# Optimization experiments

Measured on AMD Instinct MI355X. Metric: run time of the kernel, lower is better.

The kernel has to match this reference:

```python
import jax, jax.numpy as jnp
import numpy as np

B, L, H, O, N = 64, 2048, 128, 128, 256  # batch, window, num_states, num_actions, dynamics state dim


def setup_inputs() -> dict:
    key = jax.random.key(0)
    ks = jax.random.split(key, 12)
    # LRU-style stable init: |lambda| in (r_min, r_max)
    u1 = jax.random.uniform(ks[0], (N,))
    u2 = jax.random.uniform(ks[1], (N,))
    r_min, r_max = 0.4, 0.99
    nu_log = jnp.log(-0.5 * jnp.log(u1 * (r_max**2 - r_min**2) + r_min**2))
    theta_log = jnp.log(u2 * 2.0 * jnp.pi)
    lam_abs2 = jnp.exp(-2.0 * jnp.exp(nu_log))
    gamma_log = 0.5 * jnp.log(1.0 - lam_abs2)  # gamma normalization
    return {
        "state": jax.random.normal(ks[2], (B, H), jnp.float32),
        "dynamics_input_time_window": jax.random.normal(ks[3], (B, L, H), jnp.float32),
        "dynamics_disturbance_time_window": jax.random.normal(ks[4], (B, L, H), jnp.float32),
        "nu_log": nu_log.astype(jnp.float32),
        "theta_log": theta_log.astype(jnp.float32),
        "gamma_log": gamma_log.astype(jnp.float32),
        "B_re": jax.random.normal(ks[5], (N, H), jnp.float32) / np.sqrt(2 * H),
        "B_im": jax.random.normal(ks[6], (N, H), jnp.float32) / np.sqrt(2 * H),
        "C_re": jax.random.normal(ks[7], (O, N), jnp.float32) / np.sqrt(N),
        "C_im": jax.random.normal(ks[8], (O, N), jnp.float32) / np.sqrt(N),
        "D": jax.random.normal(ks[9], (O, H), jnp.float32) / np.sqrt(H),
    }


def _ssm_scan(u, nu_log, theta_log, gamma_log, B_re, B_im, C_re, C_im, D):
    # u: [B, L, H] real. Diagonal complex LRU: x_t = lam * x_{t-1} + gamma*B u_t; y = Re(C x) + D u
    lam = jnp.exp(-jnp.exp(nu_log) + 1j * jnp.exp(theta_log))           # [N]
    Bmat = (B_re + 1j * B_im) * jnp.exp(gamma_log)[:, None]              # [N, H]
    Bu = jnp.einsum("blh,nh->bln", u.astype(jnp.complex64), Bmat)       # [B, L, N]
    lam_seq = jnp.broadcast_to(lam, Bu.shape)

    def comb(e1, e2):
        a1, b1 = e1
        a2, b2 = e2
        return a1 * a2, a2 * b1 + b2

    _, x = jax.lax.associative_scan(comb, (lam_seq, Bu), axis=1)        # [B, L, N]
    y = jnp.einsum("bln,on->blo", x, C_re + 1j * C_im).real
    y = y + jnp.einsum("blh,oh->blo", u, D)
    return y


def reference(state, dynamics_input_time_window, dynamics_disturbance_time_window,
              nu_log, theta_log, gamma_log, B_re, B_im, C_re, C_im, D):
    # 3-dim branch of Actor.forward: run SSM over the disturbance window, take last step
    y = _ssm_scan(dynamics_disturbance_time_window, nu_log, theta_log, gamma_log,
                  B_re, B_im, C_re, C_im, D)                             # [B, L, O]
    action = y[:, -1, :]                                                 # [B, O]
    return action
```

## Files before the change

### kernel.cpp

```cpp
#include <hip/hip_runtime.h>
#include <hip/hip_bf16.h>
#include <math.h>
#include <stdint.h>

#define B_ 64
#define L_ 2048
#define H_ 128
#define O_ 128
#define N_ 256
#define CH_ 128
#define NCH_ 16
#define SPC_ 8

using f32x4 = __attribute__((ext_vector_type(4))) float;
using i32x4 = __attribute__((ext_vector_type(4))) int;
using h16x8 = __attribute__((ext_vector_type(8))) _Float16;

__device__ __forceinline__ unsigned short f16_bits(float v) {
    _Float16 h = (_Float16)v;
    return __builtin_bit_cast(unsigned short, h);
}
__device__ __forceinline__ int pack_f16(float a, float b) {
    return (int)((unsigned)f16_bits(a) | ((unsigned)f16_bits(b) << 16));
}

__global__ void prep_kernel(const float* __restrict__ nu_log, const float* __restrict__ theta_log,
                            const float* __restrict__ gamma_log, const float* __restrict__ B_re,
                            const float* __restrict__ B_im, unsigned short* __restrict__ B2Tr,
                            float2* __restrict__ lamjR, float2* __restrict__ lam16R,
                            float2* __restrict__ lamCCr, float* __restrict__ nuR,
                            int* __restrict__ perm, float* __restrict__ X) {
    __shared__ float nu_s[N_];
    __shared__ int perm_s[N_];
    const int t = threadIdx.x;
    float nu = expf(nu_log[t]);
    nu_s[t] = nu;
    __syncthreads();
    {
        int rank = 0;
        for (int j = 0; j < N_; ++j) {
            float vj = nu_s[j];
            rank += (vj < nu || (vj == nu && j < t)) ? 1 : 0;
        }
        perm_s[rank] = t;
    }
    __syncthreads();
    const int bb = blockIdx.x;
    if (bb < 64) {
        #pragma unroll
        for (int kk = 0; kk < 4; ++kk) {
            int e = bb * 1024 + kk * 256 + t;
            int part = e >> 15, rank = (e >> 7) & 255, h = e & 127;
            int n = perm_s[rank];
            float g = expf(gamma_log[n]);
            float v = (part ? B_im : B_re)[n * H_ + h] * g;
            B2Tr[e] = f16_bits(v);
        }
    } else if (bb == 64) {
        int r = t, n = perm_s[r];
        float nun = nu_s[n];
        double th = (double)expf(theta_log[n]);
        double rr = exp(-(double)nun);
        double sn, cs;
        sincos(th, &sn, &cs);
        double lre = rr * cs, lim = rr * sn;
        double pre = 1.0, pim = 0.0;
        for (int k = 0; k < 16; ++k) {
            lamjR[r * 16 + 15 - k] = make_float2((float)pre, (float)pim);
            double t1 = pre * lre - pim * lim, t2 = pre * lim + pim * lre;
            pre = t1; pim = t2;
        }
        lam16R[r] = make_float2((float)pre, (float)pim);
        nuR[r] = nun;
        perm[r] = n;
        double wre = pre, wim = pim;
        for (int i = 0; i < 3; ++i) {
            double a = wre * wre - wim * wim, b2 = 2.0 * wre * wim;
            wre = a; wim = b2;
        }
        double are = 1.0, aim = 0.0;
        for (int c = 15; c >= 0; --c) {
            lamCCr[c * N_ + r] = make_float2((float)are, (float)aim);
            double a = are * wre - aim * wim, b2 = are * wim + aim * wre;
            are = a; aim = b2;
        }
    } else {
        int idx = (bb - 65) * 1024 + t * 4;
        f32x4 z = {0.f, 0.f, 0.f, 0.f};
        *(f32x4*)&X[idx] = z;
    }
}

__global__ __launch_bounds__(256, 2)
void scan_kernel(const float* __restrict__ u, const unsigned short* __restrict__ B2Tr,
                 const float2* __restrict__ lamjR, const float2* __restrict__ lam16R,
                 const float2* __restrict__ lamCCr, const float* __restrict__ nuR,
                 const int* __restrict__ perm, float* __restrict__ X) {
    const int half = blockIdx.x & 1;
    const int c = (blockIdx.x >> 1) & 15;
    const int b = (int)(blockIdx.x >> 5);
    const int tid = threadIdx.x;
    const int wave = tid >> 6, lane = tid & 63;
    const int m = lane & 15, q = lane >> 4;
    const int g = half * 4 + wave;

    const float base_e = 2032.0f - 128.0f * (float)c;
    int sblk = (int)ceilf((base_e - 35.0f / nuR[half * 128]) * 0.0625f);
    if (sblk >= SPC_) return;
    if (sblk < 0) sblk = 0;
    int sp0 = (int)ceilf((base_e - 35.0f / nuR[g * 32]) * 0.0625f);
    if (sp0 < 0) sp0 = 0;
    int sp1 = (int)ceilf((base_e - 35.0f / nuR[g * 32 + 16]) * 0.0625f);
    if (sp1 < 0) sp1 = 0;

    __shared__ __align__(16) unsigned short ubuf[2][16 * 128];

    h16x8 bf[2][2][4];
    float2 wl[2][4];
    float2 l16[2];
    #pragma unroll
    for (int p = 0; p < 2; ++p) {
        const int rank = g * 32 + p * 16 + m;
        #pragma unroll
        for (int part = 0; part < 2; ++part) {
            const unsigned short* rp = B2Tr + (size_t)(part * N_ + rank) * H_ + q * 8;
            #pragma unroll
            for (int sl = 0; sl < 4; ++sl)
                bf[p][part][sl] = *(const h16x8*)(rp + sl * 32);
        }
        #pragma unroll
        for (int r = 0; r < 4; ++r) wl[p][r] = lamjR[rank * 16 + q * 4 + r];
        l16[p] = lam16R[rank];
    }

    float2 zr[2], zi[2];
    #pragma unroll
    for (int p = 0; p < 2; ++p) { zr[p] = make_float2(0.f, 0.f); zi[p] = make_float2(0.f, 0.f); }

    const int sr = tid >> 4, sg = tid & 15;
    const float* gsrc = u + ((size_t)b * L_ + (size_t)c * CH_) * H_;
    const float* gstage = gsrc + (size_t)sr * H_ + sg * 8;
    unsigned short* lwr = &ubuf[0][0] + sr * 128 + ((sg ^ sr) * 8);
    const int bufStride = 16 * 128;

    {
        const float* p4 = gstage + (size_t)sblk * 16 * H_;
        float4 a = *(const float4*)p4, b4 = *(const float4*)(p4 + 4);
        i32x4 w;
        w[0] = pack_f16(a.x, a.y);  w[1] = pack_f16(a.z, a.w);
        w[2] = pack_f16(b4.x, b4.y); w[3] = pack_f16(b4.z, b4.w);
        *(i32x4*)(lwr + (sblk & 1) * bufStride) = w;
    }
    __syncthreads();

    for (int s = sblk; s < SPC_; ++s) {
        const bool pf = (s + 1 < SPC_);
        float4 a, b4;
        if (pf) {
            const float* p4 = gstage + (size_t)(s + 1) * 16 * H_;
            a = *(const float4*)p4;
            b4 = *(const float4*)(p4 + 4);
        }

        const unsigned short* lb = &ubuf[s & 1][0];
        h16x8 afr[4];
        #pragma unroll
        for (int sl = 0; sl < 4; ++sl) {
            const int unit = (sl * 4 + q) ^ m;
            afr[sl] = *(const h16x8*)(lb + m * 128 + unit * 8);
        }

        #pragma unroll
        for (int p = 0; p < 2; ++p) {
            const int sp = p ? sp1 : sp0;
            if (s < sp) continue;
            float2 t0 = zr[p];
            zr[p].x = l16[p].x * t0.x - l16[p].y * t0.y;
            zr[p].y = l16[p].x * t0.y + l16[p].y * t0.x;
            float2 t1 = zi[p];
            zi[p].x = l16[p].x * t1.x - l16[p].y * t1.y;
            zi[p].y = l16[p].x * t1.y + l16[p].y * t1.x;
            f32x4 acc = {0.f, 0.f, 0.f, 0.f};
            #pragma unroll
            for (int sl = 0; sl < 4; ++sl)
                acc = __builtin_amdgcn_mfma_f32_16x16x32_f16(afr[sl], bf[p][0][sl], acc, 0, 0, 0);
            #pragma unroll
            for (int r = 0; r < 4; ++r) {
                zr[p].x += wl[p][r].x * acc[r];
                zr[p].y += wl[p][r].y * acc[r];
            }
            f32x4 acc2 = {0.f, 0.f, 0.f, 0.f};
            #pragma unroll
            for (int sl = 0; sl < 4; ++sl)
                acc2 = __builtin_amdgcn_mfma_f32_16x16x32_f16(afr[sl], bf[p][1][sl], acc2, 0, 0, 0);
            #pragma unroll
            for (int r = 0; r < 4; ++r) {
                zi[p].x += wl[p][r].x * acc2[r];
                zi[p].y += wl[p][r].y * acc2[r];
            }
        }

        if (pf) {
            i32x4 w;
            w[0] = pack_f16(a.x, a.y);  w[1] = pack_f16(a.z, a.w);
            w[2] = pack_f16(b4.x, b4.y); w[3] = pack_f16(b4.z, b4.w);
            *(i32x4*)(lwr + ((s + 1) & 1) * bufStride) = w;
        }
        __syncthreads();
    }

    #pragma unroll
    for (int p = 0; p < 2; ++p) {
        const int sp = p ? sp1 : sp0;
        if (sp >= SPC_) continue;
        float a = zr[p].x, b2 = zr[p].y, c2 = zi[p].x, d2 = zi[p].y;
        a  += __shfl_xor(a, 16);  a  += __shfl_xor(a, 32);
        b2 += __shfl_xor(b2, 16); b2 += __shfl_xor(b2, 32);
        c2 += __shfl_xor(c2, 16); c2 += __shfl_xor(c2, 32);
        d2 += __shfl_xor(d2, 16); d2 += __shfl_xor(d2, 32);
        if (lane < 16) {
            const int rank = g * 32 + p * 16 + m;
            const int n = perm[rank];
            float2 lc = lamCCr[c * N_ + rank];
            float prr = lc.x * a - lc.y * b2;
            float pri = lc.x * b2 + lc.y * a;
            float pir = lc.x * c2 - lc.y * d2;
            float pii = lc.x * d2 + lc.y * c2;
            atomicAdd(&X[(size_t)(b * N_ + n) * 2 + 0], prr - pii);
            atomicAdd(&X[(size_t)(b * N_ + n) * 2 + 1], pri + pir);
        }
    }
}

__global__ void out_kernel(const float* __restrict__ X, const float* __restrict__ C_re,
                           const float* __restrict__ C_im, const float* __restrict__ Dm,
                           const float* __restrict__ u, float* __restrict__ out) {
    __shared__ float xre[N_], xim[N_], ul[H_];
    const int b = blockIdx.x;
    const int t = threadIdx.x;
    xre[t] = X[(size_t)(b * N_ + t) * 2 + 0];
    xim[t] = X[(size_t)(b * N_ + t) * 2 + 1];
    if (t < H_) ul[t] = u[((size_t)b * L_ + (L_ - 1)) * H_ + t];
    __syncthreads();
    const int o = t >> 1;
    const int h = t & 1;
    const float* cre = C_re + o * N_ + h * 128;
    const float* cim = C_im + o * N_ + h * 128;
    const float* xr = xre + h * 128;
    const float* xi = xim + h * 128;
    float s = 0.f;
    #pragma unroll 4
    for (int n = 0; n < 128; ++n) s += cre[n] * xr[n] - cim[n] * xi[n];
    const float* dp = Dm + o * H_ + h * 64;
    const float* up = ul + h * 64;
    #pragma unroll 4
    for (int k = 0; k < 64; ++k) s += dp[k] * up[k];
    s += __shfl_xor(s, 1);
    if (h == 0) out[b * O_ + o] = s;
}

extern "C" void kernel_launch(void* const* d_in, const int* in_sizes, int n_in,
                              void* d_out, int out_size, void* d_ws, size_t ws_size,
                              hipStream_t stream) {
    const float* u         = (const float*)d_in[2];
    const float* nu_log    = (const float*)d_in[3];
    const float* theta_log = (const float*)d_in[4];
    const float* gamma_log = (const float*)d_in[5];
    const float* B_re      = (const float*)d_in[6];
    const float* B_im      = (const float*)d_in[7];
    const float* C_re      = (const float*)d_in[8];
    const float* C_im      = (const float*)d_in[9];
    const float* Dm        = (const float*)d_in[10];

    char* ws = (char*)d_ws;
    float*          X      = (float*)ws;
    unsigned short* B2Tr   = (unsigned short*)(ws + 131072);
    float2*         lamjR  = (float2*)(ws + 262144);
    float2*         lam16R = (float2*)(ws + 294912);
    float2*         lamCCr = (float2*)(ws + 296960);
    float*          nuR    = (float*)(ws + 329728);
    int*            perm   = (int*)(ws + 330752);

    prep_kernel<<<97, 256, 0, stream>>>(nu_log, theta_log, gamma_log, B_re, B_im,
                                        B2Tr, lamjR, lam16R, lamCCr, nuR, perm, X);
    scan_kernel<<<B_ * NCH_ * 2, 256, 0, stream>>>(u, B2Tr, lamjR, lam16R, lamCCr, nuR, perm, X);
    out_kernel<<<B_, 256, 0, stream>>>(X, C_re, C_im, Dm, u, (float*)d_out);
}
```

Before: 193.4 us.

## Deepen global prefetch to three stages with register ring and raise occupancy bound

```diff
diff --git a/kernel.cpp b/kernel.cpp
--- a/kernel.cpp
+++ b/kernel.cpp
@@ -91,7 +91,7 @@
     }
 }
 
-__global__ __launch_bounds__(256, 2)
+__global__ __launch_bounds__(256, 3)
 void scan_kernel(const float* __restrict__ u, const unsigned short* __restrict__ B2Tr,
                  const float2* __restrict__ lamjR, const float2* __restrict__ lam16R,
                  const float2* __restrict__ lamCCr, const float* __restrict__ nuR,
@@ -112,6 +112,7 @@
     if (sp0 < 0) sp0 = 0;
     int sp1 = (int)ceilf((base_e - 35.0f / nuR[g * 32 + 16]) * 0.0625f);
     if (sp1 < 0) sp1 = 0;
+    const int live = SPC_ - sblk;
 
     __shared__ __align__(16) unsigned short ubuf[2][16 * 128];
 
@@ -138,31 +139,38 @@
     for (int p = 0; p < 2; ++p) { zr[p] = make_float2(0.f, 0.f); zi[p] = make_float2(0.f, 0.f); }
 
     const int sr = tid >> 4, sg = tid & 15;
-    const float* gsrc = u + ((size_t)b * L_ + (size_t)c * CH_) * H_;
-    const float* gstage = gsrc + (size_t)sr * H_ + sg * 8;
+    const float* gbase = u + ((size_t)b * L_ + (size_t)(c * CH_ + sblk * 16)) * H_
+                           + (size_t)sr * H_ + sg * 8;
     unsigned short* lwr = &ubuf[0][0] + sr * 128 + ((sg ^ sr) * 8);
     const int bufStride = 16 * 128;
 
+    float4 ra[3], rb[3];
+    #pragma unroll
+    for (int k = 0; k < 3; ++k) {
+        if (k < live) {
+            const float* p4 = gbase + (size_t)k * 16 * H_;
+            ra[k] = *(const float4*)p4;
+            rb[k] = *(const float4*)(p4 + 4);
+        }
+    }
     {
-        const float* p4 = gstage + (size_t)sblk * 16 * H_;
-        float4 a = *(const float4*)p4, b4 = *(const float4*)(p4 + 4);
         i32x4 w;
-        w[0] = pack_f16(a.x, a.y);  w[1] = pack_f16(a.z, a.w);
-        w[2] = pack_f16(b4.x, b4.y); w[3] = pack_f16(b4.z, b4.w);
-        *(i32x4*)(lwr + (sblk & 1) * bufStride) = w;
-    }
-    __syncthreads();
-
-    for (int s = sblk; s < SPC_; ++s) {
-        const bool pf = (s + 1 < SPC_);
-        float4 a, b4;
-        if (pf) {
-            const float* p4 = gstage + (size_t)(s + 1) * 16 * H_;
-            a = *(const float4*)p4;
-            b4 = *(const float4*)(p4 + 4);
-        }
-
-        const unsigned short* lb = &ubuf[s & 1][0];
+        w[0] = pack_f16(ra[0].x, ra[0].y);  w[1] = pack_f16(ra[0].z, ra[0].w);
+        w[2] = pack_f16(rb[0].x, rb[0].y);  w[3] = pack_f16(rb[0].z, rb[0].w);
+        *(i32x4*)lwr = w;
+    }
+    __syncthreads();
+
+    #pragma unroll
+    for (int i = 0; i < SPC_; ++i) {
+        if (i >= live) break;
+        if (i + 3 < live) {
+            const float* p4 = gbase + (size_t)(i + 3) * 16 * H_;
+            ra[(i + 3) % 3] = *(const float4*)p4;
+            rb[(i + 3) % 3] = *(const float4*)(p4 + 4);
+        }
+
+        const unsigned short* lb = &ubuf[i & 1][0];
         h16x8 afr[4];
         #pragma unroll
         for (int sl = 0; sl < 4; ++sl) {
@@ -170,6 +178,15 @@
             afr[sl] = *(const h16x8*)(lb + m * 128 + unit * 8);
         }
 
+        if (i + 1 < live) {
+            const int sl3 = (i + 1) % 3;
+            i32x4 w;
+            w[0] = pack_f16(ra[sl3].x, ra[sl3].y);  w[1] = pack_f16(ra[sl3].z, ra[sl3].w);
+            w[2] = pack_f16(rb[sl3].x, rb[sl3].y);  w[3] = pack_f16(rb[sl3].z, rb[sl3].w);
+            *(i32x4*)(lwr + ((i + 1) & 1) * bufStride) = w;
+        }
+
+        const int s = sblk + i;
         #pragma unroll
         for (int p = 0; p < 2; ++p) {
             const int sp = p ? sp1 : sp0;
@@ -198,13 +215,6 @@
                 zi[p].x += wl[p][r].x * acc2[r];
                 zi[p].y += wl[p][r].y * acc2[r];
             }
-        }
-
-        if (pf) {
-            i32x4 w;
-            w[0] = pack_f16(a.x, a.y);  w[1] = pack_f16(a.z, a.w);
-            w[2] = pack_f16(b4.x, b4.y); w[3] = pack_f16(b4.z, b4.w);
-            *(i32x4*)(lwr + ((s + 1) & 1) * bufStride) = w;
         }
         __syncthreads();
     }
```

Measured after the change: 197.0 us. About the same (+1.9%).

## Deepen global-load prefetch in scan kernel, remap block order, raise occupancy

Applied to the files above, without the earlier changes.

```diff
diff --git a/kernel.cpp b/kernel.cpp
--- a/kernel.cpp
+++ b/kernel.cpp
@@ -23,6 +23,8 @@
 __device__ __forceinline__ int pack_f16(float a, float b) {
     return (int)((unsigned)f16_bits(a) | ((unsigned)f16_bits(b) << 16));
 }
+
+#define BAR_LDS() asm volatile("s_waitcnt lgkmcnt(0)\n\ts_barrier" ::: "memory")
 
 __global__ void prep_kernel(const float* __restrict__ nu_log, const float* __restrict__ theta_log,
                             const float* __restrict__ gamma_log, const float* __restrict__ B_re,
@@ -91,14 +93,15 @@
     }
 }
 
-__global__ __launch_bounds__(256, 2)
+__global__ __launch_bounds__(256, 4)
 void scan_kernel(const float* __restrict__ u, const unsigned short* __restrict__ B2Tr,
                  const float2* __restrict__ lamjR, const float2* __restrict__ lam16R,
                  const float2* __restrict__ lamCCr, const float* __restrict__ nuR,
                  const int* __restrict__ perm, float* __restrict__ X) {
-    const int half = blockIdx.x & 1;
-    const int c = (blockIdx.x >> 1) & 15;
-    const int b = (int)(blockIdx.x >> 5);
+    const int bx = blockIdx.x;
+    const int half = bx >> 10;
+    const int c = (bx >> 6) & 15;
+    const int b = bx & 63;
     const int tid = threadIdx.x;
     const int wave = tid >> 6, lane = tid & 63;
     const int m = lane & 15, q = lane >> 4;
@@ -112,6 +115,7 @@
     if (sp0 < 0) sp0 = 0;
     int sp1 = (int)ceilf((base_e - 35.0f / nuR[g * 32 + 16]) * 0.0625f);
     if (sp1 < 0) sp1 = 0;
+    const int live = SPC_ - sblk;
 
     __shared__ __align__(16) unsigned short ubuf[2][16 * 128];
 
@@ -138,38 +142,27 @@
     for (int p = 0; p < 2; ++p) { zr[p] = make_float2(0.f, 0.f); zi[p] = make_float2(0.f, 0.f); }
 
     const int sr = tid >> 4, sg = tid & 15;
-    const float* gsrc = u + ((size_t)b * L_ + (size_t)c * CH_) * H_;
-    const float* gstage = gsrc + (size_t)sr * H_ + sg * 8;
+    const float* gbase = u + ((size_t)b * L_ + (size_t)(c * CH_ + sblk * 16)) * H_
+                           + (size_t)sr * H_ + sg * 8;
     unsigned short* lwr = &ubuf[0][0] + sr * 128 + ((sg ^ sr) * 8);
     const int bufStride = 16 * 128;
 
-    {
-        const float* p4 = gstage + (size_t)sblk * 16 * H_;
-        float4 a = *(const float4*)p4, b4 = *(const float4*)(p4 + 4);
-        i32x4 w;
-        w[0] = pack_f16(a.x, a.y);  w[1] = pack_f16(a.z, a.w);
-        w[2] = pack_f16(b4.x, b4.y); w[3] = pack_f16(b4.z, b4.w);
-        *(i32x4*)(lwr + (sblk & 1) * bufStride) = w;
-    }
-    __syncthreads();
-
-    for (int s = sblk; s < SPC_; ++s) {
-        const bool pf = (s + 1 < SPC_);
-        float4 a, b4;
-        if (pf) {
-            const float* p4 = gstage + (size_t)(s + 1) * 16 * H_;
-            a = *(const float4*)p4;
-            b4 = *(const float4*)(p4 + 4);
-        }
-
-        const unsigned short* lb = &ubuf[s & 1][0];
+    float4 a0, b0, a1, b1, a2, b2;
+
+#define LOADS(slot, idx) { const float* p4_ = gbase + (size_t)(idx) * (16 * H_); \
+        a##slot = *(const float4*)p4_; b##slot = *(const float4*)(p4_ + 4); }
+#define STORES(slot, bufi) { i32x4 w_; \
+        w_[0] = pack_f16(a##slot.x, a##slot.y);  w_[1] = pack_f16(a##slot.z, a##slot.w); \
+        w_[2] = pack_f16(b##slot.x, b##slot.y);  w_[3] = pack_f16(b##slot.z, b##slot.w); \
+        *(i32x4*)(lwr + (bufi) * bufStride) = w_; }
+
+    auto compute = [&](const unsigned short* lb, int s) {
         h16x8 afr[4];
         #pragma unroll
         for (int sl = 0; sl < 4; ++sl) {
             const int unit = (sl * 4 + q) ^ m;
             afr[sl] = *(const h16x8*)(lb + m * 128 + unit * 8);
         }
-
         #pragma unroll
         for (int p = 0; p < 2; ++p) {
             const int sp = p ? sp1 : sp0;
@@ -199,15 +192,33 @@
                 zi[p].y += wl[p][r].y * acc2[r];
             }
         }
-
-        if (pf) {
-            i32x4 w;
-            w[0] = pack_f16(a.x, a.y);  w[1] = pack_f16(a.z, a.w);
-            w[2] = pack_f16(b4.x, b4.y); w[3] = pack_f16(b4.z, b4.w);
-            *(i32x4*)(lwr + ((s + 1) & 1) * bufStride) = w;
-        }
-        __syncthreads();
-    }
+    };
+
+    LOADS(0, 0);
+    if (1 < live) LOADS(1, 1);
+    if (2 < live) LOADS(2, 2);
+    STORES(0, 0);
+    BAR_LDS();
+
+#define ITER(i, lslot, wslot) \
+    if ((i) < live) { \
+        if ((i) + 3 < live) LOADS(lslot, (i) + 3); \
+        if ((i) + 1 < live) STORES(wslot, ((i) + 1) & 1); \
+        compute(&ubuf[(i) & 1][0], sblk + (i)); \
+        BAR_LDS(); \
+    }
+
+    ITER(0, 0, 1)
+    ITER(1, 1, 2)
+    ITER(2, 2, 0)
+    ITER(3, 0, 1)
+    ITER(4, 1, 2)
+    ITER(5, 2, 0)
+    ITER(6, 0, 1)
+    ITER(7, 1, 2)
+#undef ITER
+#undef LOADS
+#undef STORES
 
     #pragma unroll
     for (int p = 0; p < 2; ++p) {
```

Result: slower. 238.2 us (+23.2%).

## Stage whole chunk in LDS once and run per-wave independent scans

Applied to the files above, without the earlier changes.

```diff
diff --git a/kernel.cpp b/kernel.cpp
--- a/kernel.cpp
+++ b/kernel.cpp
@@ -91,143 +91,118 @@
     }
 }
 
-__global__ __launch_bounds__(256, 2)
+__global__ __launch_bounds__(512, 4)
 void scan_kernel(const float* __restrict__ u, const unsigned short* __restrict__ B2Tr,
                  const float2* __restrict__ lamjR, const float2* __restrict__ lam16R,
                  const float2* __restrict__ lamCCr, const float* __restrict__ nuR,
                  const int* __restrict__ perm, float* __restrict__ X) {
-    const int half = blockIdx.x & 1;
-    const int c = (blockIdx.x >> 1) & 15;
-    const int b = (int)(blockIdx.x >> 5);
+    const int bx = blockIdx.x;
+    const int c = bx & 15;
+    const int b = bx >> 4;
     const int tid = threadIdx.x;
-    const int wave = tid >> 6, lane = tid & 63;
+
+    __shared__ __align__(16) unsigned short Asm[CH_ * H_];
+
+    {
+        const int r = tid >> 2;
+        const int qq = tid & 3;
+        const float* gsrc = u + ((size_t)b * L_ + (size_t)(c * CH_ + r)) * H_ + qq * 32;
+        f32x4 Lv[8];
+        #pragma unroll
+        for (int k = 0; k < 8; ++k) Lv[k] = *(const f32x4*)(gsrc + k * 4);
+        #pragma unroll
+        for (int j = 0; j < 4; ++j) {
+            const int unit = (qq * 4 + j) ^ (r & 15);
+            i32x4 w;
+            w[0] = pack_f16(Lv[2 * j][0], Lv[2 * j][1]);
+            w[1] = pack_f16(Lv[2 * j][2], Lv[2 * j][3]);
+            w[2] = pack_f16(Lv[2 * j + 1][0], Lv[2 * j + 1][1]);
+            w[3] = pack_f16(Lv[2 * j + 1][2], Lv[2 * j + 1][3]);
+            *(i32x4*)&Asm[r * H_ + unit * 8] = w;
+        }
+    }
+    __syncthreads();
+
+    const int g = tid >> 6;
+    const int lane = tid & 63;
     const int m = lane & 15, q = lane >> 4;
-    const int g = half * 4 + wave;
 
     const float base_e = 2032.0f - 128.0f * (float)c;
-    int sblk = (int)ceilf((base_e - 35.0f / nuR[half * 128]) * 0.0625f);
-    if (sblk >= SPC_) return;
-    if (sblk < 0) sblk = 0;
     int sp0 = (int)ceilf((base_e - 35.0f / nuR[g * 32]) * 0.0625f);
     if (sp0 < 0) sp0 = 0;
     int sp1 = (int)ceilf((base_e - 35.0f / nuR[g * 32 + 16]) * 0.0625f);
     if (sp1 < 0) sp1 = 0;
 
-    __shared__ __align__(16) unsigned short ubuf[2][16 * 128];
-
-    h16x8 bf[2][2][4];
-    float2 wl[2][4];
-    float2 l16[2];
-    #pragma unroll
-    for (int p = 0; p < 2; ++p) {
-        const int rank = g * 32 + p * 16 + m;
-        #pragma unroll
-        for (int part = 0; part < 2; ++part) {
-            const unsigned short* rp = B2Tr + (size_t)(part * N_ + rank) * H_ + q * 8;
-            #pragma unroll
-            for (int sl = 0; sl < 4; ++sl)
-                bf[p][part][sl] = *(const h16x8*)(rp + sl * 32);
-        }
-        #pragma unroll
-        for (int r = 0; r < 4; ++r) wl[p][r] = lamjR[rank * 16 + q * 4 + r];
-        l16[p] = lam16R[rank];
-    }
-
-    float2 zr[2], zi[2];
-    #pragma unroll
-    for (int p = 0; p < 2; ++p) { zr[p] = make_float2(0.f, 0.f); zi[p] = make_float2(0.f, 0.f); }
-
-    const int sr = tid >> 4, sg = tid & 15;
-    const float* gsrc = u + ((size_t)b * L_ + (size_t)c * CH_) * H_;
-    const float* gstage = gsrc + (size_t)sr * H_ + sg * 8;
-    unsigned short* lwr = &ubuf[0][0] + sr * 128 + ((sg ^ sr) * 8);
-    const int bufStride = 16 * 128;
-
-    {
-        const float* p4 = gstage + (size_t)sblk * 16 * H_;
-        float4 a = *(const float4*)p4, b4 = *(const float4*)(p4 + 4);
-        i32x4 w;
-        w[0] = pack_f16(a.x, a.y);  w[1] = pack_f16(a.z, a.w);
-        w[2] = pack_f16(b4.x, b4.y); w[3] = pack_f16(b4.z, b4.w);
-        *(i32x4*)(lwr + (sblk & 1) * bufStride) = w;
-    }
-    __syncthreads();
-
-    for (int s = sblk; s < SPC_; ++s) {
-        const bool pf = (s + 1 < SPC_);
-        float4 a, b4;
-        if (pf) {
-            const float* p4 = gstage + (size_t)(s + 1) * 16 * H_;
-            a = *(const float4*)p4;
-            b4 = *(const float4*)(p4 + 4);
-        }
-
-        const unsigned short* lb = &ubuf[s & 1][0];
-        h16x8 afr[4];
-        #pragma unroll
-        for (int sl = 0; sl < 4; ++sl) {
-            const int unit = (sl * 4 + q) ^ m;
-            afr[sl] = *(const h16x8*)(lb + m * 128 + unit * 8);
-        }
-
+    if (sp0 < SPC_) {
         #pragma unroll
         for (int p = 0; p < 2; ++p) {
             const int sp = p ? sp1 : sp0;
-            if (s < sp) continue;
-            float2 t0 = zr[p];
-            zr[p].x = l16[p].x * t0.x - l16[p].y * t0.y;
-            zr[p].y = l16[p].x * t0.y + l16[p].y * t0.x;
-            float2 t1 = zi[p];
-            zi[p].x = l16[p].x * t1.x - l16[p].y * t1.y;
-            zi[p].y = l16[p].x * t1.y + l16[p].y * t1.x;
-            f32x4 acc = {0.f, 0.f, 0.f, 0.f};
+            if (sp >= SPC_) continue;
+            const int rank = g * 32 + p * 16 + m;
+
+            h16x8 bfr[2][4];
             #pragma unroll
-            for (int sl = 0; sl < 4; ++sl)
-                acc = __builtin_amdgcn_mfma_f32_16x16x32_f16(afr[sl], bf[p][0][sl], acc, 0, 0, 0);
+            for (int part = 0; part < 2; ++part) {
+                const unsigned short* rp = B2Tr + (size_t)(part * N_ + rank) * H_ + q * 8;
+                #pragma unroll
+                for (int sl = 0; sl < 4; ++sl)
+                    bfr[part][sl] = *(const h16x8*)(rp + sl * 32);
+            }
+            float2 wl[4];
             #pragma unroll
-            for (int r = 0; r < 4; ++r) {
-                zr[p].x += wl[p][r].x * acc[r];
-                zr[p].y += wl[p][r].y * acc[r];
+            for (int r2 = 0; r2 < 4; ++r2) wl[r2] = lamjR[rank * 16 + q * 4 + r2];
+            const float2 l16 = lam16R[rank];
+
+            float2 zre = make_float2(0.f, 0.f), zim = make_float2(0.f, 0.f);
+            for (int s = sp; s < SPC_; ++s) {
+                const int row = s * 16 + m;
+                h16x8 afr[4];
+                #pragma unroll
+                for (int sl = 0; sl < 4; ++sl) {
+                    const int unit = (sl * 4 + q) ^ m;
+                    afr[sl] = *(const h16x8*)&Asm[row * H_ + unit * 8];
+                }
+                float2 t0 = zre;
+                zre.x = l16.x * t0.x - l16.y * t0.y;
+                zre.y = l16.x * t0.y + l16.y * t0.x;
+                float2 t1 = zim;
+                zim.x = l16.x * t1.x - l16.y * t1.y;
+                zim.y = l16.x * t1.y + l16.y * t1.x;
+                f32x4 acc = {0.f, 0.f, 0.f, 0.f};
+                #pragma unroll
+                for (int sl = 0; sl < 4; ++sl)
+                    acc = __builtin_amdgcn_mfma_f32_16x16x32_f16(afr[sl], bfr[0][sl], acc, 0, 0, 0);
+                #pragma unroll
+                for (int r2 = 0; r2 < 4; ++r2) {
+                    zre.x += wl[r2].x * acc[r2];
+                    zre.y += wl[r2].y * acc[r2];
+                }
+                f32x4 acc2 = {0.f, 0.f, 0.f, 0.f};
+                #pragma unroll
+                for (int sl = 0; sl < 4; ++sl)
+                    acc2 = __builtin_amdgcn_mfma_f32_16x16x32_f16(afr[sl], bfr[1][sl], acc2, 0, 0, 0);
+                #pragma unroll
+                for (int r2 = 0; r2 < 4; ++r2) {
+                    zim.x += wl[r2].x * acc2[r2];
+                    zim.y += wl[r2].y * acc2[r2];
+                }
             }
-            f32x4 acc2 = {0.f, 0.f, 0.f, 0.f};
-            #pragma unroll
-            for (int sl = 0; sl < 4; ++sl)
-                acc2 = __builtin_amdgcn_mfma_f32_16x16x32_f16(afr[sl], bf[p][1][sl], acc2, 0, 0, 0);
-            #pragma unroll
-            for (int r = 0; r < 4; ++r) {
-                zi[p].x += wl[p][r].x * acc2[r];
-                zi[p].y += wl[p][r].y * acc2[r];
+
+            float a = zre.x, b2 = zre.y, c2 = zim.x, d2 = zim.y;
+            a  += __shfl_xor(a, 16);  a  += __shfl_xor(a, 32);
+            b2 += __shfl_xor(b2, 16); b2 += __shfl_xor(b2, 32);
+            c2 += __shfl_xor(c2, 16); c2 += __shfl_xor(c2, 32);
+            d2 += __shfl_xor(d2, 16); d2 += __shfl_xor(d2, 32);
+            if (lane < 16) {
+                const int n = perm[rank];
+                float2 lc = lamCCr[c * N_ + rank];
+                float prr = lc.x * a - lc.y * b2;
+                float pri = lc.x * b2 + lc.y * a;
+                float pir = lc.x * c2 - lc.y * d2;
+                float pii = lc.x * d2 + lc.y * c2;
+                atomicAdd(&X[(size_t)(b * N_ + n) * 2 + 0], prr - pii);
+                atomicAdd(&X[(size_t)(b * N_ + n) * 2 + 1], pri + pir);
             }
-        }
-
-        if (pf) {
-            i32x4 w;
-            w[0] = pack_f16(a.x, a.y);  w[1] = pack_f16(a.z, a.w);
-            w[2] = pack_f16(b4.x, b4.y); w[3] = pack_f16(b4.z, b4.w);
-            *(i32x4*)(lwr + ((s + 1) & 1) * bufStride) = w;
-        }
-        __syncthreads();
-    }
-
-    #pragma unroll
-    for (int p = 0; p < 2; ++p) {
-        const int sp = p ? sp1 : sp0;
-        if (sp >= SPC_) continue;
-        float a = zr[p].x, b2 = zr[p].y, c2 = zi[p].x, d2 = zi[p].y;
-        a  += __shfl_xor(a, 16);  a  += __shfl_xor(a, 32);
-        b2 += __shfl_xor(b2, 16); b2 += __shfl_xor(b2, 32);
-        c2 += __shfl_xor(c2, 16); c2 += __shfl_xor(c2, 32);
-        d2 += __shfl_xor(d2, 16); d2 += __shfl_xor(d2, 32);
-        if (lane < 16) {
-            const int rank = g * 32 + p * 16 + m;
-            const int n = perm[rank];
-            float2 lc = lamCCr[c * N_ + rank];
-            float prr = lc.x * a - lc.y * b2;
-            float pri = lc.x * b2 + lc.y * a;
-            float pir = lc.x * c2 - lc.y * d2;
-            float pii = lc.x * d2 + lc.y * c2;
-            atomicAdd(&X[(size_t)(b * N_ + n) * 2 + 0], prr - pii);
-            atomicAdd(&X[(size_t)(b * N_ + n) * 2 + 1], pri + pir);
         }
     }
 }
@@ -283,6 +258,6 @@
 
     prep_kernel<<<97, 256, 0, stream>>>(nu_log, theta_log, gamma_log, B_re, B_im,
                                         B2Tr, lamjR, lam16R, lamCCr, nuR, perm, X);
-    scan_kernel<<<B_ * NCH_ * 2, 256, 0, stream>>>(u, B2Tr, lamjR, lam16R, lamCCr, nuR, perm, X);
+    scan_kernel<<<B_ * NCH_, 512, 0, stream>>>(u, B2Tr, lamjR, lam16R, lamCCr, nuR, perm, X);
     out_kernel<<<B_, 256, 0, stream>>>(X, C_re, C_im, Dm, u, (float*)d_out);
 }
```

After: 186.5 us. 1.04x faster.
